# Kernel tuning notes

Measured on AMD Instinct MI355X. Metric: run time of the kernel, lower is better.

Reference implementation:

```python
import jax, jax.numpy as jnp
import numpy as np

T, N, K, E = 5, 2048, 20, 512
H, AI, BL, G1, G2, U = 64, 32, 64, 64, 64, 8
SLOPE, ALPHA = 0.01, 1.0


def gru(x, Wih, Whh, bih, bhh):
    # batch_first torch nn.GRU with h0 = 0. x: [B, L, I] -> [B, L, Hd]
    Hd = Whh.shape[1]
    def step(h, xt):
        gi = xt @ Wih.T + bih
        gh = h @ Whh.T + bhh
        ir, iz, in_ = jnp.split(gi, 3, axis=-1)
        hr, hz, hn = jnp.split(gh, 3, axis=-1)
        r = jax.nn.sigmoid(ir + hr)
        z = jax.nn.sigmoid(iz + hz)
        n = jnp.tanh(in_ + r * hn)
        h_new = (1.0 - z) * n + z * h
        return h_new, h_new
    h0 = jnp.zeros((x.shape[0], Hd), x.dtype)
    _, ys = jax.lax.scan(step, h0, jnp.swapaxes(x, 0, 1))
    return jnp.swapaxes(ys, 0, 1)


def lin_attn(x, w1, b1, w2):
    # LinearAttention: softmax over dim=2 (weights_size=1), then bmm -> [B,1,H]
    inter = jnp.tanh(x @ w1.T + b1)
    w = jax.nn.softmax(inter @ w2.T, axis=2)  # [B,L,1]
    return jnp.einsum('blk,blh->bkh', w, x)


def sgat_multi(x, W, a, adj):
    # All U SGAT heads at once. Decompose a^T [Wh_i || Wh_j] = s1_i + s2_j
    # (same math as the dense NxNx2F construction, without materializing it).
    O = W.shape[-1]
    Wh = jnp.einsum('nf,ufo->uno', x, W)                 # [U,N,O]
    s1 = jnp.einsum('uno,uo->un', Wh, a[:, :O, 0])
    s2 = jnp.einsum('uno,uo->un', Wh, a[:, O:, 0])
    e = jax.nn.leaky_relu(s1[:, :, None] + s2[:, None, :], SLOPE)  # [U,N,N]
    e = jnp.where(adj[None, :, :] > 0, e, -9e15)
    att = jax.nn.softmax(e, axis=2)
    h = jnp.einsum('unm,umo->uno', att, Wh)              # [U,N,O]
    # torch.cat over heads along feature dim -> [N, U*O]
    return jnp.transpose(h, (1, 0, 2)).reshape(x.shape[0], -1)


def setup_inputs() -> dict:
    key = jax.random.key(0)
    ks = iter(jax.random.split(key, 40))
    def nrm(shape, scale=0.1):
        return jax.random.normal(next(ks), shape, dtype=jnp.float32) * scale
    d = {}
    d['p'] = nrm((N, T, 3), 1.0)
    d['m'] = nrm((T, N, K, E), 1.0)
    adj = (jax.random.uniform(next(ks), (N, N)) < 0.05).astype(jnp.float32)
    d['adj'] = jnp.maximum(adj, jnp.eye(N, dtype=jnp.float32))
    d['Wih_p'] = nrm((3 * H, 3)); d['Whh_p'] = nrm((3 * H, H))
    d['bih_p'] = nrm((3 * H,)); d['bhh_p'] = nrm((3 * H,))
    d['Wih_m'] = nrm((3 * H, E)); d['Whh_m'] = nrm((3 * H, H))
    d['bih_m'] = nrm((3 * H,)); d['bhh_m'] = nrm((3 * H,))
    d['Wih_s'] = nrm((3 * H, H)); d['Whh_s'] = nrm((3 * H, H))
    d['bih_s'] = nrm((3 * H,)); d['bhh_s'] = nrm((3 * H,))
    for pref in ('ap', 'am', 'as'):
        d[pref + '_w1'] = nrm((AI, H)); d[pref + '_b1'] = nrm((AI,))
        d[pref + '_w2'] = nrm((1, AI))
    d['blend_W'] = nrm((BL, H, H)); d['blend_b'] = nrm((BL,))
    d['g1_W'] = nrm((U, BL, G1)); d['g1_a'] = nrm((U, 2 * G1, 1))
    d['g2_W'] = nrm((U, U * G1, G2)); d['g2_a'] = nrm((U, 2 * G2, 1))
    d['fin_W'] = nrm((1, U * G2)); d['fin_b'] = nrm((1,))
    return d


def reference(p, m, adj, Wih_p, Whh_p, bih_p, bhh_p, Wih_m, Whh_m, bih_m, bhh_m,
              Wih_s, Whh_s, bih_s, bhh_s, ap_w1, ap_b1, ap_w2, am_w1, am_b1, am_w2,
              as_w1, as_b1, as_w2, blend_W, blend_b, g1_W, g1_a, g2_W, g2_a,
              fin_W, fin_b):
    h_p = gru(p, Wih_p, Whh_p, bih_p, bhh_p)                     # [N,T,H]
    q = lin_attn(h_p, ap_w1, ap_b1, ap_w2)                       # [N,1,H]
    # all T message-days through gru_m at once (equivalent to python loop)
    h_m = gru(m.reshape(T * N, K, E), Wih_m, Whh_m, bih_m, bhh_m)
    r = lin_attn(h_m, am_w1, am_b1, am_w2).reshape(T, N, H).transpose(1, 0, 2)
    h_s = gru(r, Wih_s, Whh_s, bih_s, bhh_s)                     # [N,T,H]
    c = lin_attn(h_s, as_w1, as_b1, as_w2)                       # [N,1,H]
    # Blend: bilinear + relu
    x = jax.nn.relu(jnp.einsum('nbi,oij,nbj->nbo', q, blend_W, c) + blend_b)
    x = x.reshape(N, BL)
    z = jax.nn.elu(sgat_multi(x, g1_W, g1_a, adj), ALPHA)        # [N,U*G1]
    new_z = jax.nn.sigmoid(sgat_multi(z, g2_W, g2_a, adj))       # [N,U*G2]
    return jax.nn.sigmoid(new_z @ fin_W.T + fin_b)               # [N,1]
```

## Files before the change

kernel.cpp:

```cpp
#include <hip/hip_runtime.h>
#include <math.h>

namespace {

constexpr int T = 5, N = 2048, K = 20, E = 512;
constexpr int H = 64, U = 8;
constexpr int CAP = 512;
constexpr float SLOPE = 0.01f;

typedef __attribute__((ext_vector_type(8))) short short8;
typedef __attribute__((ext_vector_type(4))) float f32x4;

__device__ inline float sigm(float x) { return 1.0f / (1.0f + expf(-x)); }

__device__ inline void bsplit(float x, short& hi, short& lo) {
  unsigned u = __float_as_uint(x);
  hi = (short)(u >> 16);
  float r = x - __uint_as_float(u & 0xFFFF0000u);
  lo = (short)(__float_as_uint(r) >> 16);
}

__device__ inline float rdlane(float v, int lane) {
  return __int_as_float(__builtin_amdgcn_readlane(__float_as_int(v), lane));
}

__device__ inline void pack512(const float* __restrict__ src, short* __restrict__ dst,
                               const int Ksz, const int pb, const int nPB) {
  const int nb64 = Ksz >> 6;
  const int total = 8 * Ksz * 64;
  for (int idx = threadIdx.x + pb * 256; idx < total; idx += 256 * nPB) {
    const int u = idx / (Ksz * 64), rem = idx - u * Ksz * 64;
    const int f = rem >> 6, o = rem & 63;
    const int col = u * 64 + o;
    const long base = ((long)(col >> 7) * nb64 + (f >> 6)) * 8192
                    + (((f >> 5) & 1) * 8 + ((col >> 4) & 7)) * 512
                    + ((f >> 3) & 3) * 128 + (col & 15) * 8 + (f & 7);
    dst[base] = (short)(__float_as_uint(src[idx]) >> 16);
  }
}

__global__ __launch_bounds__(256) void k_prep_all(
    const float* __restrict__ WihM, const float* __restrict__ WhhM,
    const float* __restrict__ WihS, const float* __restrict__ WhhS,
    const float* __restrict__ WhhP, const float* __restrict__ Wb,
    const float* __restrict__ g1W, const float* __restrict__ g2W,
    const float* __restrict__ adj,
    const float* __restrict__ p, const float* __restrict__ WihP,
    const float* __restrict__ bihP, const float* __restrict__ bhhP,
    short* __restrict__ BfM, short* __restrict__ BfS,
    short* __restrict__ Bf1, short* __restrict__ Bf2,
    float* __restrict__ WhhTm, float* __restrict__ WhhTs,
    float* __restrict__ Wt2, int* __restrict__ nbr, int* __restrict__ deg,
    float* __restrict__ q)
{
  const int b = blockIdx.x;
  if (b < N / 4) {
    const int w = threadIdx.x >> 6, lane = threadIdx.x & 63;
    const int i = b * 4 + w;
    int base = 0;
    for (int j0 = 0; j0 < N; j0 += 64) {
      const float v = adj[(long)i * N + j0 + lane];
      const unsigned long long mask = __ballot(v > 0.f);
      const int pre = __popcll(mask & ((1ull << lane) - 1ull));
      if (v > 0.f && base + pre < CAP) nbr[i * CAP + base + pre] = j0 + lane;
      base += __popcll(mask);
    }
    if (lane == 0) deg[i] = base < CAP ? base : CAP;
    return;
  }
  if (b < N / 4 + 128) {
    const int pb = b - N / 4;
    constexpr int NPB = 128;
    for (int idx = threadIdx.x + pb * 256; idx < 192 * 512; idx += 256 * NPB) {
      const int o = idx >> 9, k = idx & 511;
      const long base = (long)(k >> 6) * 12288 + (((k >> 5) & 1) * 12 + (o >> 4)) * 512
                      + ((k >> 3) & 3) * 128 + (o & 15) * 8 + (k & 7);
      BfM[base] = (short)(__float_as_uint(WihM[idx]) >> 16);
    }
    for (int idx = threadIdx.x + pb * 256; idx < 192 * 64; idx += 256 * NPB) {
      const int o = idx >> 6, k = idx & 63;
      const long base = (((k >> 5) & 1) * 12 + (o >> 4)) * 512
                      + ((k >> 3) & 3) * 128 + (o & 15) * 8 + (k & 7);
      BfS[base] = (short)(__float_as_uint(WihS[idx]) >> 16);
    }
    for (int idx = threadIdx.x + pb * 256; idx < 64 * 192; idx += 256 * NPB) {
      const int k2 = idx / 192, row = idx % 192;
      WhhTm[idx] = WhhM[row * 64 + k2];
      WhhTs[idx] = WhhS[row * 64 + k2];
    }
    for (int idx = threadIdx.x + pb * 256; idx < 64 * 64 * 64; idx += 256 * NPB) {
      const int o = idx >> 12, rem = idx & 4095, i = rem >> 6, j = rem & 63;
      Wt2[((i * 16 + (j >> 2)) * 64 + o) * 4 + (j & 3)] = Wb[(o * 64 + i) * 64 + j];
    }
    pack512(g1W, Bf1, 64, pb, NPB);
    pack512(g2W, Bf2, 512, pb, NPB);
    return;
  }
  const int rb = b - (N / 4 + 128);
  const int w = threadIdx.x >> 6, l = threadIdx.x & 63;
  const int n = rb * 4 + w;
  float wr[64], wz[64], wn[64];
  #pragma unroll
  for (int k2 = 0; k2 < 64; ++k2) {
    wr[k2] = WhhP[l * 64 + k2];
    wz[k2] = WhhP[(64 + l) * 64 + k2];
    wn[k2] = WhhP[(128 + l) * 64 + k2];
  }
  float iR[3], iZ[3], iN[3];
  #pragma unroll
  for (int c = 0; c < 3; ++c) {
    iR[c] = WihP[l * 3 + c];
    iZ[c] = WihP[(64 + l) * 3 + c];
    iN[c] = WihP[(128 + l) * 3 + c];
  }
  const float biR = bihP[l], biZ = bihP[64 + l], biN = bihP[128 + l];
  const float bhR = bhhP[l], bhZ = bhhP[64 + l], bhN = bhhP[128 + l];
  float h = 0.f, qs = 0.f;
  for (int t = 0; t < T; ++t) {
    const float x0 = p[n * 15 + t * 3], x1 = p[n * 15 + t * 3 + 1], x2 = p[n * 15 + t * 3 + 2];
    const float gR = biR + iR[0] * x0 + iR[1] * x1 + iR[2] * x2;
    const float gZ = biZ + iZ[0] * x0 + iZ[1] * x1 + iZ[2] * x2;
    const float gN = biN + iN[0] * x0 + iN[1] * x1 + iN[2] * x2;
    float aR = bhR, aZ = bhZ, aN = bhN;
    #pragma unroll
    for (int k2 = 0; k2 < 64; ++k2) {
      const float hk = rdlane(h, k2);
      aR += wr[k2] * hk; aZ += wz[k2] * hk; aN += wn[k2] * hk;
    }
    const float r = sigm(gR + aR), z = sigm(gZ + aZ);
    const float nn = tanhf(gN + r * aN);
    h = (1.f - z) * nn + z * h;
    qs += h;
  }
  q[n * H + l] = qs;
}

__global__ __launch_bounds__(256, 2) void k_gemm(
    const float* __restrict__ A, const short* __restrict__ Bf,
    const float* __restrict__ bias, float* __restrict__ out,
    const long row0, const int nb, const int strideA)
{
  __shared__ alignas(16) short Bc[2][24 * 512];
  const int tid = threadIdx.x, w = tid >> 6, l = tid & 63;
  const int lr = l & 15, g = l >> 4;
  const long blkrow = (long)blockIdx.x * 128;

  f32x4 acc[2][12];
  #pragma unroll
  for (int mf = 0; mf < 2; ++mf)
    #pragma unroll
    for (int nt = 0; nt < 12; ++nt) acc[mf][nt] = (f32x4){0.f, 0.f, 0.f, 0.f};

  float4 pf[2][2][2];

  auto LOADA = [&](int b) {
    #pragma unroll
    for (int kc = 0; kc < 2; ++kc)
      #pragma unroll
      for (int mf = 0; mf < 2; ++mf) {
        const long r = blkrow + w * 32 + mf * 16 + lr;
        const float* __restrict__ src = A + (row0 + r) * (long)strideA + b * 64 + kc * 32 + g * 8;
        pf[kc][mf][0] = *reinterpret_cast<const float4*>(src);
        pf[kc][mf][1] = *reinterpret_cast<const float4*>(src + 4);
      }
  };
  auto STAGE = [&](int buf, int b) {
    const short* __restrict__ bsrc = Bf + (long)b * 12288;
    #pragma unroll
    for (int i = 0; i < 6; ++i) {
      const int c = w + i * 4;
      __builtin_amdgcn_global_load_lds(
          (const __attribute__((address_space(1))) void*)(bsrc + c * 512 + l * 8),
          (__attribute__((address_space(3))) void*)(&Bc[buf][c * 512]), 16, 0, 0);
    }
  };

  STAGE(0, 0);
  LOADA(0);
  __syncthreads();

  for (int b = 0; b < nb; ++b) {
    const bool more = (b + 1 < nb);
    if (more) STAGE((b + 1) & 1, b + 1);
    short8 ah[2][2], al[2][2];
    #pragma unroll
    for (int kc = 0; kc < 2; ++kc)
      #pragma unroll
      for (int mf = 0; mf < 2; ++mf) {
        const float4 v0 = pf[kc][mf][0], v1 = pf[kc][mf][1];
        short h0,l0,h1,l1,h2,l2,h3,l3,h4,l4,h5,l5,h6,l6,h7,l7;
        bsplit(v0.x,h0,l0); bsplit(v0.y,h1,l1); bsplit(v0.z,h2,l2); bsplit(v0.w,h3,l3);
        bsplit(v1.x,h4,l4); bsplit(v1.y,h5,l5); bsplit(v1.z,h6,l6); bsplit(v1.w,h7,l7);
        ah[kc][mf] = (short8){h0,h1,h2,h3,h4,h5,h6,h7};
        al[kc][mf] = (short8){l0,l1,l2,l3,l4,l5,l6,l7};
      }
    if (more) LOADA(b + 1);
    const short* __restrict__ bcur = &Bc[b & 1][0];
    #pragma unroll
    for (int kc = 0; kc < 2; ++kc) {
      #pragma unroll
      for (int nt = 0; nt < 12; ++nt) {
        const short8 bh = *reinterpret_cast<const short8*>(bcur + (kc * 12 + nt) * 512 + l * 8);
        #pragma unroll
        for (int mf = 0; mf < 2; ++mf) {
          acc[mf][nt] = __builtin_amdgcn_mfma_f32_16x16x32_bf16(ah[kc][mf], bh, acc[mf][nt], 0, 0, 0);
          acc[mf][nt] = __builtin_amdgcn_mfma_f32_16x16x32_bf16(al[kc][mf], bh, acc[mf][nt], 0, 0, 0);
        }
      }
    }
    __syncthreads();
  }

  #pragma unroll
  for (int mf = 0; mf < 2; ++mf) {
    const long rbase = blkrow + w * 32 + mf * 16 + g * 4;
    #pragma unroll
    for (int nt = 0; nt < 12; ++nt) {
      const int col = nt * 16 + lr;
      const float bb = bias[col];
      #pragma unroll
      for (int i = 0; i < 4; ++i)
        out[(rbase + i) * 192 + col] = acc[mf][nt][i] + bb;
    }
  }
}

__global__ __launch_bounds__(256, 3) void k_gemmW(
    const float* __restrict__ A, const short* __restrict__ Bf2,
    const float* __restrict__ ga,
    float* __restrict__ Wh, float* __restrict__ s1, float* __restrict__ s2,
    const int nb, const int strideA)
{
  __shared__ alignas(16) short Bc[2][16 * 512];
  const int tid = threadIdx.x, w = tid >> 6, l = tid & 63;
  const int lr = l & 15, g = l >> 4;
  const long blkrow = (long)blockIdx.x * 64;
  const int cb = blockIdx.y;

  f32x4 acc[8];
  #pragma unroll
  for (int nt = 0; nt < 8; ++nt) acc[nt] = (f32x4){0.f, 0.f, 0.f, 0.f};

  float4 pf[2][2];

  auto LOADA = [&](int b) {
    #pragma unroll
    for (int kc = 0; kc < 2; ++kc) {
      const long r = blkrow + w * 16 + lr;
      const float* __restrict__ src = A + r * (long)strideA + b * 64 + kc * 32 + g * 8;
      pf[kc][0] = *reinterpret_cast<const float4*>(src);
      pf[kc][1] = *reinterpret_cast<const float4*>(src + 4);
    }
  };
  auto STAGE = [&](int buf, int b) {
    const short* __restrict__ bsrc = Bf2 + ((long)cb * nb + b) * 8192;
    #pragma unroll
    for (int i = 0; i < 4; ++i) {
      const int c = w + i * 4;
      __builtin_amdgcn_global_load_lds(
          (const __attribute__((address_space(1))) void*)(bsrc + c * 512 + l * 8),
          (__attribute__((address_space(3))) void*)(&Bc[buf][c * 512]), 16, 0, 0);
    }
  };

  STAGE(0, 0);
  LOADA(0);
  __syncthreads();

  for (int b = 0; b < nb; ++b) {
    const bool more = (b + 1 < nb);
    if (more) STAGE((b + 1) & 1, b + 1);
    short8 ah[2], al[2];
    #pragma unroll
    for (int kc = 0; kc < 2; ++kc) {
      const float4 v0 = pf[kc][0], v1 = pf[kc][1];
      short h0,l0,h1,l1,h2,l2,h3,l3,h4,l4,h5,l5,h6,l6,h7,l7;
      bsplit(v0.x,h0,l0); bsplit(v0.y,h1,l1); bsplit(v0.z,h2,l2); bsplit(v0.w,h3,l3);
      bsplit(v1.x,h4,l4); bsplit(v1.y,h5,l5); bsplit(v1.z,h6,l6); bsplit(v1.w,h7,l7);
      ah[kc] = (short8){h0,h1,h2,h3,h4,h5,h6,h7};
      al[kc] = (short8){l0,l1,l2,l3,l4,l5,l6,l7};
    }
    if (more) LOADA(b + 1);
    const short* __restrict__ bcur = &Bc[b & 1][0];
    #pragma unroll
    for (int kc = 0; kc < 2; ++kc) {
      #pragma unroll
      for (int nt = 0; nt < 8; ++nt) {
        const short8 bh = *reinterpret_cast<const short8*>(bcur + (kc * 8 + nt) * 512 + l * 8);
        acc[nt] = __builtin_amdgcn_mfma_f32_16x16x32_bf16(ah[kc], bh, acc[nt], 0, 0, 0);
        acc[nt] = __builtin_amdgcn_mfma_f32_16x16x32_bf16(al[kc], bh, acc[nt], 0, 0, 0);
      }
    }
    __syncthreads();
  }

  const long rbase = blkrow + w * 16 + g * 4;
  #pragma unroll
  for (int nt = 0; nt < 8; ++nt) {
    const int col = cb * 128 + nt * 16 + lr;
    const int u = col >> 6, o = col & 63;
    #pragma unroll
    for (int i = 0; i < 4; ++i)
      Wh[((long)u * N + (rbase + i)) * 64 + o] = acc[nt][i];
  }
  #pragma unroll
  for (int i = 0; i < 4; ++i) {
    const long r = rbase + i;
    #pragma unroll
    for (int uh = 0; uh < 2; ++uh) {
      const int u = cb * 2 + uh;
      float p1 = 0.f, p2 = 0.f;
      #pragma unroll
      for (int nt4 = 0; nt4 < 4; ++nt4) {
        const float v = acc[uh * 4 + nt4][i];
        const int o = nt4 * 16 + lr;
        p1 += v * ga[u * 128 + o];
        p2 += v * ga[u * 128 + 64 + o];
      }
      #pragma unroll
      for (int dd = 8; dd > 0; dd >>= 1) { p1 += __shfl_xor(p1, dd, 64); p2 += __shfl_xor(p2, dd, 64); }
      if (lr == 0) { s1[u * N + r] = p1; s2[u * N + r] = p2; }
    }
  }
}

__global__ __launch_bounds__(256, 2) void k_recur(
    const float* __restrict__ gi, const float* __restrict__ WhhT,
    const float* __restrict__ bhh, float* __restrict__ rout, const int seq0)
{
  const int tid = threadIdx.x, w = tid >> 6, l = tid & 63;
  const int lseq = blockIdx.x * 4 + w;
  float wr[64], wz[64], wn[64];
  #pragma unroll
  for (int k2 = 0; k2 < 64; ++k2) {
    wr[k2] = WhhT[k2 * 192 + l];
    wz[k2] = WhhT[k2 * 192 + 64 + l];
    wn[k2] = WhhT[k2 * 192 + 128 + l];
  }
  const float bR = bhh[l], bZ = bhh[64 + l], bN = bhh[128 + l];
  const float* __restrict__ grow = gi + (long)lseq * K * 192;
  float h = 0.f, rsum = 0.f;
  float gR = grow[l], gZ = grow[64 + l], gN = grow[128 + l];
  for (int k = 0; k < K; ++k) {
    float nR = 0.f, nZ = 0.f, nN = 0.f;
    if (k + 1 < K) {
      const int off = (k + 1) * 192;
      nR = grow[off + l]; nZ = grow[off + 64 + l]; nN = grow[off + 128 + l];
    }
    float aR = bR, aZ = bZ, aN = bN;
    #pragma unroll
    for (int k2 = 0; k2 < 64; ++k2) {
      const float hk = rdlane(h, k2);
      aR += wr[k2] * hk; aZ += wz[k2] * hk; aN += wn[k2] * hk;
    }
    const float r = sigm(gR + aR);
    const float z = sigm(gZ + aZ);
    const float nn = tanhf(gN + r * aN);
    h = (1.f - z) * nn + z * h;
    rsum += h;
    gR = nR; gZ = nZ; gN = nN;
  }
  const int gseq = seq0 + lseq;
  const int tt = gseq / N, n = gseq % N;
  rout[(n * T + tt) * H + l] = rsum;
}

__global__ __launch_bounds__(256, 2) void k_recur_s(
    const float* __restrict__ gx, const float* __restrict__ WhhT,
    const float* __restrict__ bhh, float* __restrict__ c)
{
  const int tid = threadIdx.x, w = tid >> 6, l = tid & 63;
  const int n = blockIdx.x * 4 + w;
  float wr[64], wz[64], wn[64];
  #pragma unroll
  for (int k2 = 0; k2 < 64; ++k2) {
    wr[k2] = WhhT[k2 * 192 + l];
    wz[k2] = WhhT[k2 * 192 + 64 + l];
    wn[k2] = WhhT[k2 * 192 + 128 + l];
  }
  const float bR = bhh[l], bZ = bhh[64 + l], bN = bhh[128 + l];
  const float* __restrict__ grow = gx + (long)n * T * 192;
  float h = 0.f, cs = 0.f;
  for (int t = 0; t < T; ++t) {
    const float gR = grow[t * 192 + l], gZ = grow[t * 192 + 64 + l], gN = grow[t * 192 + 128 + l];
    float aR = bR, aZ = bZ, aN = bN;
    #pragma unroll
    for (int k2 = 0; k2 < 64; ++k2) {
      const float hk = rdlane(h, k2);
      aR += wr[k2] * hk; aZ += wz[k2] * hk; aN += wn[k2] * hk;
    }
    const float r = sigm(gR + aR), z = sigm(gZ + aZ);
    const float nn = tanhf(gN + r * aN);
    h = (1.f - z) * nn + z * h;
    cs += h;
  }
  c[n * H + l] = cs;
}

__global__ __launch_bounds__(256) void k_blend(
    const float* __restrict__ q, const float* __restrict__ c,
    const float* __restrict__ Wt2, const float* __restrict__ b,
    float* __restrict__ xout)
{
  __shared__ float qs[8][64];
  __shared__ alignas(16) float cs[8][64];
  const int tid = threadIdx.x;
  const int o = tid & 63, grp = tid >> 6;
  const int n0 = blockIdx.x * 8;
  for (int idx = tid; idx < 512; idx += 256) {
    qs[idx >> 6][idx & 63] = q[(n0 + (idx >> 6)) * 64 + (idx & 63)];
    cs[idx >> 6][idx & 63] = c[(n0 + (idx >> 6)) * 64 + (idx & 63)];
  }
  __syncthreads();
  const int na = grp * 2, nb = na + 1;
  float acca = b[o], accb = b[o];
  const float4* __restrict__ W4 = reinterpret_cast<const float4*>(Wt2);
  const float4* ca4 = reinterpret_cast<const float4*>(&cs[na][0]);
  const float4* cb4 = reinterpret_cast<const float4*>(&cs[nb][0]);
  for (int i = 0; i < 64; ++i) {
    float pa = 0.f, pb = 0.f;
    #pragma unroll
    for (int j4 = 0; j4 < 16; ++j4) {
      const float4 wv = W4[(i * 16 + j4) * 64 + o];
      const float4 va = ca4[j4], vb = cb4[j4];
      pa += wv.x * va.x + wv.y * va.y + wv.z * va.z + wv.w * va.w;
      pb += wv.x * vb.x + wv.y * vb.y + wv.z * vb.z + wv.w * vb.w;
    }
    acca += qs[na][i] * pa;
    accb += qs[nb][i] * pb;
  }
  xout[(n0 + na) * 64 + o] = fmaxf(acca, 0.f);
  xout[(n0 + nb) * 64 + o] = fmaxf(accb, 0.f);
}

__global__ __launch_bounds__(256) void k_gat_attn(
    const float* __restrict__ Wh, const float* __restrict__ s1,
    const float* __restrict__ s2, const int* __restrict__ nbr,
    const int* __restrict__ deg, const int mode, float* __restrict__ out)
{
  __shared__ float ew[4][CAP];
  __shared__ int nb[4][CAP];
  const int w = threadIdx.x >> 6, lane = threadIdx.x & 63;
  const int row = blockIdx.x * 4 + w;
  const int u = row >> 11;
  const int i = row & (N - 1);
  const int d = deg[i];
  const float su = s1[u * N + i];
  float mx = -1e30f;
  for (int t = lane; t < d; t += 64) {
    const int j = nbr[i * CAP + t];
    float e = su + s2[u * N + j];
    e = e > 0.f ? e : SLOPE * e;
    ew[w][t] = e; nb[w][t] = j;
    mx = fmaxf(mx, e);
  }
  #pragma unroll
  for (int dd = 32; dd > 0; dd >>= 1) mx = fmaxf(mx, __shfl_xor(mx, dd, 64));
  float sm = 0.f;
  for (int t = lane; t < d; t += 64) {
    const float ex = expf(ew[w][t] - mx);
    ew[w][t] = ex;
    sm += ex;
  }
  #pragma unroll
  for (int dd = 32; dd > 0; dd >>= 1) sm += __shfl_xor(sm, dd, 64);
  __syncthreads();
  const float inv = 1.f / sm;
  float a0 = 0.f, a1 = 0.f, a2 = 0.f, a3 = 0.f;
  const float* __restrict__ whb = Wh + (long)u * N * 64 + lane;
  int t = 0;
  for (; t + 4 <= d; t += 4) {
    const float e0 = ew[w][t],     e1 = ew[w][t + 1];
    const float e2 = ew[w][t + 2], e3 = ew[w][t + 3];
    const int j0 = nb[w][t],     j1 = nb[w][t + 1];
    const int j2 = nb[w][t + 2], j3 = nb[w][t + 3];
    a0 += e0 * whb[(long)j0 * 64];
    a1 += e1 * whb[(long)j1 * 64];
    a2 += e2 * whb[(long)j2 * 64];
    a3 += e3 * whb[(long)j3 * 64];
  }
  for (; t < d; ++t) a0 += ew[w][t] * whb[(long)nb[w][t] * 64];
  float acc = ((a0 + a1) + (a2 + a3)) * inv;
  float val;
  if (mode == 0) val = acc > 0.f ? acc : (expf(acc) - 1.f);
  else           val = 1.f / (1.f + expf(-acc));
  out[(long)i * (U * 64) + u * 64 + lane] = val;
}

__global__ __launch_bounds__(256) void k_final(
    const float* __restrict__ nz, const float* __restrict__ fw,
    const float* __restrict__ fb, float* __restrict__ out)
{
  const int w = threadIdx.x >> 6, lane = threadIdx.x & 63;
  const int n = blockIdx.x * 4 + w;
  float p = 0.f;
  #pragma unroll
  for (int f = lane; f < 512; f += 64) p += nz[(long)n * 512 + f] * fw[f];
  #pragma unroll
  for (int d = 32; d > 0; d >>= 1) p += __shfl_xor(p, d, 64);
  if (lane == 0) out[n] = 1.f / (1.f + expf(-(p + fb[0])));
}

}

extern "C" void kernel_launch(void* const* d_in, const int* in_sizes, int n_in,
                              void* d_out, int out_size, void* d_ws, size_t ws_size,
                              hipStream_t stream)
{
  const float* p     = (const float*)d_in[0];
  const float* m     = (const float*)d_in[1];
  const float* adj   = (const float*)d_in[2];
  const float* Wih_p = (const float*)d_in[3];
  const float* Whh_p = (const float*)d_in[4];
  const float* bih_p = (const float*)d_in[5];
  const float* bhh_p = (const float*)d_in[6];
  const float* Wih_m = (const float*)d_in[7];
  const float* Whh_m = (const float*)d_in[8];
  const float* bih_m = (const float*)d_in[9];
  const float* bhh_m = (const float*)d_in[10];
  const float* Wih_s = (const float*)d_in[11];
  const float* Whh_s = (const float*)d_in[12];
  const float* bih_s = (const float*)d_in[13];
  const float* bhh_s = (const float*)d_in[14];
  const float* blend_W = (const float*)d_in[24];
  const float* blend_b = (const float*)d_in[25];
  const float* g1W = (const float*)d_in[26];
  const float* g1a = (const float*)d_in[27];
  const float* g2W = (const float*)d_in[28];
  const float* g2a = (const float*)d_in[29];
  const float* finW = (const float*)d_in[30];
  const float* finb = (const float*)d_in[31];

  float* ws = (float*)d_ws;
  float* q    = ws;
  float* rr   = q + N * H;
  float* c    = rr + N * T * H;
  float* xb   = c + N * H;
  float* Wh1  = xb + N * H;
  float* s1a  = Wh1 + U * N * 64;
  float* s2a  = s1a + U * N;
  float* z    = s2a + U * N;
  float* Wh2  = z + (long)N * 512;
  float* s1b  = Wh2 + U * N * 64;
  float* s2b  = s1b + U * N;
  float* nz   = s2b + U * N;
  float* Wt2  = nz + (long)N * 512;
  float* gx   = Wt2 + 64 * 64 * 64;
  float* WhhTm = gx + (long)10240 * 192;
  float* WhhTs = WhhTm + 64 * 192;
  int*   nbr  = (int*)(WhhTs + 64 * 192);
  int*   deg  = nbr + (long)N * CAP;
  short* BfM  = (short*)(deg + N);
  short* BfS  = BfM + 8 * 12288;
  short* Bf1  = BfS + 12288;
  short* Bf2  = Bf1 + 4 * 8192;
  float* gi   = (float*)(Bf2 + 4 * 8 * 8192);

  const long avail = (long)(ws_size / 4) - (gi - ws);
  const long total_seqs = (long)T * N;
  long chunk = (avail / ((long)K * 192) / 32) * 32;
  if (chunk > total_seqs) chunk = total_seqs;
  if (chunk < 32) chunk = 32;

  k_prep_all<<<N / 4 + 128 + N / 4, 256, 0, stream>>>(
      Wih_m, Whh_m, Wih_s, Whh_s, Whh_p, blend_W, g1W, g2W, adj,
      p, Wih_p, bih_p, bhh_p,
      BfM, BfS, Bf1, Bf2, WhhTm, WhhTs, Wt2, nbr, deg, q);
  for (long s0 = 0; s0 < total_seqs; s0 += chunk) {
    const long cs = (total_seqs - s0) < chunk ? (total_seqs - s0) : chunk;
    const long rows = cs * K;
    k_gemm<<<(int)(rows / 128), 256, 0, stream>>>(m, BfM, bih_m, gi, s0 * K, 8, 512);
    k_recur<<<(int)(cs / 4), 256, 0, stream>>>(gi, WhhTm, bhh_m, rr, (int)s0);
  }
  k_gemm<<<80, 256, 0, stream>>>(rr, BfS, bih_s, gx, 0, 1, 64);
  k_recur_s<<<N / 4, 256, 0, stream>>>(gx, WhhTs, bhh_s, c);
  k_blend<<<N / 8, 256, 0, stream>>>(q, c, Wt2, blend_b, xb);
  k_gemmW<<<dim3(N / 64, 4), 256, 0, stream>>>(xb, Bf1, g1a, Wh1, s1a, s2a, 1, 64);
  k_gat_attn<<<(U * N) / 4, 256, 0, stream>>>(Wh1, s1a, s2a, nbr, deg, 0, z);
  k_gemmW<<<dim3(N / 64, 4), 256, 0, stream>>>(z, Bf2, g2a, Wh2, s1b, s2b, 8, 512);
  k_gat_attn<<<(U * N) / 4, 256, 0, stream>>>(Wh2, s1b, s2b, nbr, deg, 1, nz);
  k_final<<<N / 4, 256, 0, stream>>>(nz, finW, finb, (float*)d_out);
}
```

Baseline: 449.8 us.

## Fuse GRU input-projection GEMM with recurrence in one kernel per block

Merges the MFMA input-projection GEMM and the GRU recurrence into a single templated kernel. Each block computes 160 rows (8 message sequences or 32 stock sequences), writes gi, syncs, and then runs the recurrence on those rows while they are likely still in cache. This removes separate kernel launches and the global round-trip between kernels. The cost is uneven MFMA tiles per wave (3/3/2/2) and a recurrence phase that carries the GEMM kernel's register and LDS footprint, which may lower occupancy and serialise GEMM and recurrence work within each block.

```diff
diff --git a/kernel.cpp b/kernel.cpp
--- a/kernel.cpp
+++ b/kernel.cpp
@@ -135,34 +135,40 @@
   q[n * H + l] = qs;
 }
 
-__global__ __launch_bounds__(256, 2) void k_gemm(
+template<int SL>
+__global__ __launch_bounds__(256, 2) void k_gemm_recur(
     const float* __restrict__ A, const short* __restrict__ Bf,
-    const float* __restrict__ bias, float* __restrict__ out,
-    const long row0, const int nb, const int strideA)
+    const float* __restrict__ bias, float* __restrict__ gi,
+    const float* __restrict__ WhhT, const float* __restrict__ bhh,
+    float* __restrict__ outp, const long row0, const int seq0,
+    const int nb, const int strideA)
 {
   __shared__ alignas(16) short Bc[2][24 * 512];
   const int tid = threadIdx.x, w = tid >> 6, l = tid & 63;
   const int lr = l & 15, g = l >> 4;
-  const long blkrow = (long)blockIdx.x * 128;
-
-  f32x4 acc[2][12];
-  #pragma unroll
-  for (int mf = 0; mf < 2; ++mf)
+  const long blkrow = (long)blockIdx.x * 160;
+  const int t0 = (w < 2) ? w * 3 : 6 + (w - 2) * 2;
+  const int ntile = (w < 2) ? 3 : 2;
+
+  f32x4 acc[3][12];
+  #pragma unroll
+  for (int mf = 0; mf < 3; ++mf)
     #pragma unroll
     for (int nt = 0; nt < 12; ++nt) acc[mf][nt] = (f32x4){0.f, 0.f, 0.f, 0.f};
 
-  float4 pf[2][2][2];
+  float4 pf[2][3][2];
 
   auto LOADA = [&](int b) {
     #pragma unroll
     for (int kc = 0; kc < 2; ++kc)
       #pragma unroll
-      for (int mf = 0; mf < 2; ++mf) {
-        const long r = blkrow + w * 32 + mf * 16 + lr;
-        const float* __restrict__ src = A + (row0 + r) * (long)strideA + b * 64 + kc * 32 + g * 8;
-        pf[kc][mf][0] = *reinterpret_cast<const float4*>(src);
-        pf[kc][mf][1] = *reinterpret_cast<const float4*>(src + 4);
-      }
+      for (int mf = 0; mf < 3; ++mf)
+        if (mf < ntile) {
+          const long r = blkrow + (t0 + mf) * 16 + lr;
+          const float* __restrict__ src = A + (row0 + r) * (long)strideA + b * 64 + kc * 32 + g * 8;
+          pf[kc][mf][0] = *reinterpret_cast<const float4*>(src);
+          pf[kc][mf][1] = *reinterpret_cast<const float4*>(src + 4);
+        }
   };
   auto STAGE = [&](int buf, int b) {
     const short* __restrict__ bsrc = Bf + (long)b * 12288;
@@ -182,18 +188,19 @@
   for (int b = 0; b < nb; ++b) {
     const bool more = (b + 1 < nb);
     if (more) STAGE((b + 1) & 1, b + 1);
-    short8 ah[2][2], al[2][2];
+    short8 ah[2][3], al[2][3];
     #pragma unroll
     for (int kc = 0; kc < 2; ++kc)
       #pragma unroll
-      for (int mf = 0; mf < 2; ++mf) {
-        const float4 v0 = pf[kc][mf][0], v1 = pf[kc][mf][1];
-        short h0,l0,h1,l1,h2,l2,h3,l3,h4,l4,h5,l5,h6,l6,h7,l7;
-        bsplit(v0.x,h0,l0); bsplit(v0.y,h1,l1); bsplit(v0.z,h2,l2); bsplit(v0.w,h3,l3);
-        bsplit(v1.x,h4,l4); bsplit(v1.y,h5,l5); bsplit(v1.z,h6,l6); bsplit(v1.w,h7,l7);
-        ah[kc][mf] = (short8){h0,h1,h2,h3,h4,h5,h6,h7};
-        al[kc][mf] = (short8){l0,l1,l2,l3,l4,l5,l6,l7};
-      }
+      for (int mf = 0; mf < 3; ++mf)
+        if (mf < ntile) {
+          const float4 v0 = pf[kc][mf][0], v1 = pf[kc][mf][1];
+          short h0,l0,h1,l1,h2,l2,h3,l3,h4,l4,h5,l5,h6,l6,h7,l7;
+          bsplit(v0.x,h0,l0); bsplit(v0.y,h1,l1); bsplit(v0.z,h2,l2); bsplit(v0.w,h3,l3);
+          bsplit(v1.x,h4,l4); bsplit(v1.y,h5,l5); bsplit(v1.z,h6,l6); bsplit(v1.w,h7,l7);
+          ah[kc][mf] = (short8){h0,h1,h2,h3,h4,h5,h6,h7};
+          al[kc][mf] = (short8){l0,l1,l2,l3,l4,l5,l6,l7};
+        }
     if (more) LOADA(b + 1);
     const short* __restrict__ bcur = &Bc[b & 1][0];
     #pragma unroll
@@ -202,25 +209,72 @@
       for (int nt = 0; nt < 12; ++nt) {
         const short8 bh = *reinterpret_cast<const short8*>(bcur + (kc * 12 + nt) * 512 + l * 8);
         #pragma unroll
-        for (int mf = 0; mf < 2; ++mf) {
-          acc[mf][nt] = __builtin_amdgcn_mfma_f32_16x16x32_bf16(ah[kc][mf], bh, acc[mf][nt], 0, 0, 0);
-          acc[mf][nt] = __builtin_amdgcn_mfma_f32_16x16x32_bf16(al[kc][mf], bh, acc[mf][nt], 0, 0, 0);
-        }
+        for (int mf = 0; mf < 3; ++mf)
+          if (mf < ntile) {
+            acc[mf][nt] = __builtin_amdgcn_mfma_f32_16x16x32_bf16(ah[kc][mf], bh, acc[mf][nt], 0, 0, 0);
+            acc[mf][nt] = __builtin_amdgcn_mfma_f32_16x16x32_bf16(al[kc][mf], bh, acc[mf][nt], 0, 0, 0);
+          }
       }
     }
     __syncthreads();
   }
 
   #pragma unroll
-  for (int mf = 0; mf < 2; ++mf) {
-    const long rbase = blkrow + w * 32 + mf * 16 + g * 4;
-    #pragma unroll
-    for (int nt = 0; nt < 12; ++nt) {
-      const int col = nt * 16 + lr;
-      const float bb = bias[col];
-      #pragma unroll
-      for (int i = 0; i < 4; ++i)
-        out[(rbase + i) * 192 + col] = acc[mf][nt][i] + bb;
+  for (int mf = 0; mf < 3; ++mf)
+    if (mf < ntile) {
+      const long rbase = blkrow + (t0 + mf) * 16 + g * 4;
+      #pragma unroll
+      for (int nt = 0; nt < 12; ++nt) {
+        const int col = nt * 16 + lr;
+        const float bb = bias[col];
+        #pragma unroll
+        for (int i = 0; i < 4; ++i)
+          gi[(rbase + i) * 192 + col] = acc[mf][nt][i] + bb;
+      }
+    }
+  __syncthreads();
+
+  constexpr int SPW = 40 / SL;
+  float wr[64], wz[64], wn[64];
+  #pragma unroll
+  for (int k2 = 0; k2 < 64; ++k2) {
+    wr[k2] = WhhT[k2 * 192 + l];
+    wz[k2] = WhhT[k2 * 192 + 64 + l];
+    wn[k2] = WhhT[k2 * 192 + 128 + l];
+  }
+  const float bR = bhh[l], bZ = bhh[64 + l], bN = bhh[128 + l];
+  #pragma unroll 1
+  for (int ss = 0; ss < SPW; ++ss) {
+    const int lseq = w * SPW + ss;
+    const float* __restrict__ grow = gi + (blkrow + (long)lseq * SL) * 192;
+    float h = 0.f, rsum = 0.f;
+    float gR = grow[l], gZ = grow[64 + l], gN = grow[128 + l];
+    for (int k = 0; k < SL; ++k) {
+      float nR = 0.f, nZ = 0.f, nN = 0.f;
+      if (k + 1 < SL) {
+        const int off = (k + 1) * 192;
+        nR = grow[off + l]; nZ = grow[off + 64 + l]; nN = grow[off + 128 + l];
+      }
+      float aR = bR, aZ = bZ, aN = bN;
+      #pragma unroll
+      for (int k2 = 0; k2 < 64; ++k2) {
+        const float hk = rdlane(h, k2);
+        aR += wr[k2] * hk; aZ += wz[k2] * hk; aN += wn[k2] * hk;
+      }
+      const float r = sigm(gR + aR);
+      const float z = sigm(gZ + aZ);
+      const float nn = tanhf(gN + r * aN);
+      h = (1.f - z) * nn + z * h;
+      rsum += h;
+      gR = nR; gZ = nZ; gN = nN;
+    }
+    if constexpr (SL == 20) {
+      const int gseq = seq0 + (int)(blkrow / 20) + lseq;
+      const int tt = gseq / N, n = gseq % N;
+      outp[(n * T + tt) * H + l] = rsum;
+    } else {
+      const int n = (int)(blkrow / 5) + lseq;
+      outp[n * H + l] = rsum;
     }
   }
 }
@@ -322,79 +376,6 @@
       if (lr == 0) { s1[u * N + r] = p1; s2[u * N + r] = p2; }
     }
   }
-}
-
-__global__ __launch_bounds__(256, 2) void k_recur(
-    const float* __restrict__ gi, const float* __restrict__ WhhT,
-    const float* __restrict__ bhh, float* __restrict__ rout, const int seq0)
-{
-  const int tid = threadIdx.x, w = tid >> 6, l = tid & 63;
-  const int lseq = blockIdx.x * 4 + w;
-  float wr[64], wz[64], wn[64];
-  #pragma unroll
-  for (int k2 = 0; k2 < 64; ++k2) {
-    wr[k2] = WhhT[k2 * 192 + l];
-    wz[k2] = WhhT[k2 * 192 + 64 + l];
-    wn[k2] = WhhT[k2 * 192 + 128 + l];
-  }
-  const float bR = bhh[l], bZ = bhh[64 + l], bN = bhh[128 + l];
-  const float* __restrict__ grow = gi + (long)lseq * K * 192;
-  float h = 0.f, rsum = 0.f;
-  float gR = grow[l], gZ = grow[64 + l], gN = grow[128 + l];
-  for (int k = 0; k < K; ++k) {
-    float nR = 0.f, nZ = 0.f, nN = 0.f;
-    if (k + 1 < K) {
-      const int off = (k + 1) * 192;
-      nR = grow[off + l]; nZ = grow[off + 64 + l]; nN = grow[off + 128 + l];
-    }
-    float aR = bR, aZ = bZ, aN = bN;
-    #pragma unroll
-    for (int k2 = 0; k2 < 64; ++k2) {
-      const float hk = rdlane(h, k2);
-      aR += wr[k2] * hk; aZ += wz[k2] * hk; aN += wn[k2] * hk;
-    }
-    const float r = sigm(gR + aR);
-    const float z = sigm(gZ + aZ);
-    const float nn = tanhf(gN + r * aN);
-    h = (1.f - z) * nn + z * h;
-    rsum += h;
-    gR = nR; gZ = nZ; gN = nN;
-  }
-  const int gseq = seq0 + lseq;
-  const int tt = gseq / N, n = gseq % N;
-  rout[(n * T + tt) * H + l] = rsum;
-}
-
-__global__ __launch_bounds__(256, 2) void k_recur_s(
-    const float* __restrict__ gx, const float* __restrict__ WhhT,
-    const float* __restrict__ bhh, float* __restrict__ c)
-{
-  const int tid = threadIdx.x, w = tid >> 6, l = tid & 63;
-  const int n = blockIdx.x * 4 + w;
-  float wr[64], wz[64], wn[64];
-  #pragma unroll
-  for (int k2 = 0; k2 < 64; ++k2) {
-    wr[k2] = WhhT[k2 * 192 + l];
-    wz[k2] = WhhT[k2 * 192 + 64 + l];
-    wn[k2] = WhhT[k2 * 192 + 128 + l];
-  }
-  const float bR = bhh[l], bZ = bhh[64 + l], bN = bhh[128 + l];
-  const float* __restrict__ grow = gx + (long)n * T * 192;
-  float h = 0.f, cs = 0.f;
-  for (int t = 0; t < T; ++t) {
-    const float gR = grow[t * 192 + l], gZ = grow[t * 192 + 64 + l], gN = grow[t * 192 + 128 + l];
-    float aR = bR, aZ = bZ, aN = bN;
-    #pragma unroll
-    for (int k2 = 0; k2 < 64; ++k2) {
-      const float hk = rdlane(h, k2);
-      aR += wr[k2] * hk; aZ += wz[k2] * hk; aN += wn[k2] * hk;
-    }
-    const float r = sigm(gR + aR), z = sigm(gZ + aZ);
-    const float nn = tanhf(gN + r * aN);
-    h = (1.f - z) * nn + z * h;
-    cs += h;
-  }
-  c[n * H + l] = cs;
 }
 
 __global__ __launch_bounds__(256) void k_blend(
@@ -569,11 +550,11 @@
   for (long s0 = 0; s0 < total_seqs; s0 += chunk) {
     const long cs = (total_seqs - s0) < chunk ? (total_seqs - s0) : chunk;
     const long rows = cs * K;
-    k_gemm<<<(int)(rows / 128), 256, 0, stream>>>(m, BfM, bih_m, gi, s0 * K, 8, 512);
-    k_recur<<<(int)(cs / 4), 256, 0, stream>>>(gi, WhhTm, bhh_m, rr, (int)s0);
-  }
-  k_gemm<<<80, 256, 0, stream>>>(rr, BfS, bih_s, gx, 0, 1, 64);
-  k_recur_s<<<N / 4, 256, 0, stream>>>(gx, WhhTs, bhh_s, c);
+    k_gemm_recur<20><<<(int)(rows / 160), 256, 0, stream>>>(
+        m, BfM, bih_m, gi, WhhTm, bhh_m, rr, s0 * K, (int)s0, 8, 512);
+  }
+  k_gemm_recur<5><<<(N * T) / 160, 256, 0, stream>>>(
+      rr, BfS, bih_s, gx, WhhTs, bhh_s, c, 0, 0, 1, 64);
   k_blend<<<N / 8, 256, 0, stream>>>(q, c, Wt2, blend_b, xb);
   k_gemmW<<<dim3(N / 64, 4), 256, 0, stream>>>(xb, Bf1, g1a, Wh1, s1a, s2a, 1, 64);
   k_gat_attn<<<(U * N) / 4, 256, 0, stream>>>(Wh1, s1a, s2a, nbr, deg, 0, z);
```

New measurement: 516.6 us. 1.15x slower.

## Split each GAT attention row across a full 256-thread block

Applied to the files above, without the earlier changes.

The GAT attention kernel now assigns one (head,node) row per block instead of one per wavefront. The four wavefronts cooperate on the softmax through shared-memory max/sum reductions, split the neighbor aggregation in interleaved strides, and reduce partial sums through shared memory. This is meant to raise memory-level parallelism on the gathered neighbor rows, at the cost of four times as many blocks, extra barriers, and three idle wavefronts during the final write.

```diff
diff --git a/kernel.cpp b/kernel.cpp
--- a/kernel.cpp
+++ b/kernel.cpp
@@ -438,53 +438,58 @@
     const float* __restrict__ s2, const int* __restrict__ nbr,
     const int* __restrict__ deg, const int mode, float* __restrict__ out)
 {
-  __shared__ float ew[4][CAP];
-  __shared__ int nb[4][CAP];
-  const int w = threadIdx.x >> 6, lane = threadIdx.x & 63;
-  const int row = blockIdx.x * 4 + w;
+  __shared__ float ew[CAP];
+  __shared__ int nb[CAP];
+  __shared__ float red[4];
+  __shared__ float pacc[4][64];
+  const int tid = threadIdx.x, w = tid >> 6, lane = tid & 63;
+  const int row = blockIdx.x;
   const int u = row >> 11;
   const int i = row & (N - 1);
   const int d = deg[i];
   const float su = s1[u * N + i];
   float mx = -1e30f;
-  for (int t = lane; t < d; t += 64) {
+  for (int t = tid; t < d; t += 256) {
     const int j = nbr[i * CAP + t];
     float e = su + s2[u * N + j];
     e = e > 0.f ? e : SLOPE * e;
-    ew[w][t] = e; nb[w][t] = j;
+    ew[t] = e; nb[t] = j;
     mx = fmaxf(mx, e);
   }
   #pragma unroll
   for (int dd = 32; dd > 0; dd >>= 1) mx = fmaxf(mx, __shfl_xor(mx, dd, 64));
+  if (lane == 0) red[w] = mx;
+  __syncthreads();
+  mx = fmaxf(fmaxf(red[0], red[1]), fmaxf(red[2], red[3]));
+  __syncthreads();
   float sm = 0.f;
-  for (int t = lane; t < d; t += 64) {
-    const float ex = expf(ew[w][t] - mx);
-    ew[w][t] = ex;
+  for (int t = tid; t < d; t += 256) {
+    const float ex = expf(ew[t] - mx);
+    ew[t] = ex;
     sm += ex;
   }
   #pragma unroll
   for (int dd = 32; dd > 0; dd >>= 1) sm += __shfl_xor(sm, dd, 64);
-  __syncthreads();
-  const float inv = 1.f / sm;
-  float a0 = 0.f, a1 = 0.f, a2 = 0.f, a3 = 0.f;
+  if (lane == 0) red[w] = sm;
+  __syncthreads();
+  const float inv = 1.f / (red[0] + red[1] + red[2] + red[3]);
+  float a0 = 0.f, a1 = 0.f;
   const float* __restrict__ whb = Wh + (long)u * N * 64 + lane;
-  int t = 0;
-  for (; t + 4 <= d; t += 4) {
-    const float e0 = ew[w][t],     e1 = ew[w][t + 1];
-    const float e2 = ew[w][t + 2], e3 = ew[w][t + 3];
-    const int j0 = nb[w][t],     j1 = nb[w][t + 1];
-    const int j2 = nb[w][t + 2], j3 = nb[w][t + 3];
-    a0 += e0 * whb[(long)j0 * 64];
-    a1 += e1 * whb[(long)j1 * 64];
-    a2 += e2 * whb[(long)j2 * 64];
-    a3 += e3 * whb[(long)j3 * 64];
-  }
-  for (; t < d; ++t) a0 += ew[w][t] * whb[(long)nb[w][t] * 64];
-  float acc = ((a0 + a1) + (a2 + a3)) * inv;
-  float val;
-  if (mode == 0) val = acc > 0.f ? acc : (expf(acc) - 1.f);
-  else           val = 1.f / (1.f + expf(-acc));
-  out[(long)i * (U * 64) + u * 64 + lane] = val;
+  int t = w;
+  for (; t + 4 < d; t += 8) {
+    a0 += ew[t] * whb[(long)nb[t] * 64];
+    a1 += ew[t + 4] * whb[(long)nb[t + 4] * 64];
+  }
+  if (t < d) a0 += ew[t] * whb[(long)nb[t] * 64];
+  pacc[w][lane] = a0 + a1;
+  __syncthreads();
+  if (w == 0) {
+    const float acc = (pacc[0][lane] + pacc[1][lane] + pacc[2][lane] + pacc[3][lane]) * inv;
+    float val;
+    if (mode == 0) val = acc > 0.f ? acc : (expf(acc) - 1.f);
+    else           val = 1.f / (1.f + expf(-acc));
+    out[(long)i * (U * 64) + u * 64 + lane] = val;
+  }
 }
 
 __global__ __launch_bounds__(256) void k_final(
@@ -576,8 +581,8 @@
   k_recur_s<<<N / 4, 256, 0, stream>>>(gx, WhhTs, bhh_s, c);
   k_blend<<<N / 8, 256, 0, stream>>>(q, c, Wt2, blend_b, xb);
   k_gemmW<<<dim3(N / 64, 4), 256, 0, stream>>>(xb, Bf1, g1a, Wh1, s1a, s2a, 1, 64);
-  k_gat_attn<<<(U * N) / 4, 256, 0, stream>>>(Wh1, s1a, s2a, nbr, deg, 0, z);
+  k_gat_attn<<<U * N, 256, 0, stream>>>(Wh1, s1a, s2a, nbr, deg, 0, z);
   k_gemmW<<<dim3(N / 64, 4), 256, 0, stream>>>(z, Bf2, g2a, Wh2, s1b, s2b, 8, 512);
-  k_gat_attn<<<(U * N) / 4, 256, 0, stream>>>(Wh2, s1b, s2b, nbr, deg, 1, nz);
+  k_gat_attn<<<U * N, 256, 0, stream>>>(Wh2, s1b, s2b, nbr, deg, 1, nz);
   k_final<<<N / 4, 256, 0, stream>>>(nz, finW, finb, (float*)d_out);
 }
```

Result: slower. 491.6 us (+9.3%).
